# Optimization experiments

Hardware: AMD Instinct MI355X
Metric: run time of the kernel (lower is better)

## Reference

```python
import jax, jax.numpy as jnp
import numpy as np

SAMPLE_RATE = 16000
M = 10          # welch averaging window (frames)
R = 30          # long-term window (frames)
EPS = 1e-5
WIN_LEN = 25    # source bug: ms value used as window length in samples


def _hamming_sq_sum(n):
    # torch.hamming_window(n, periodic=True): 0.54 - 0.46*cos(2*pi*k/n)
    k = np.arange(n)
    w = 0.54 - 0.46 * np.cos(2.0 * np.pi * k / n)
    return np.float32((w ** 2).sum())


def _windowed_mean(x, w):
    """y[:, i, :] = mean(x[:, max(0, i-w):i, :]) for i>=1, y[:,0,:]=0.
    Vectorized via prefix sums: replaces the per-frame Python loop."""
    B, T, F = x.shape
    c = jnp.cumsum(x, axis=1)
    c = jnp.concatenate([jnp.zeros((B, 1, F), x.dtype), c], axis=1)  # c[:, i] = sum of first i frames
    idx = jnp.arange(T)
    lo = jnp.maximum(idx - w, 0)
    cnt = jnp.minimum(idx, w).astype(x.dtype)            # window length per frame (0 at i=0)
    mean = (c[:, idx] - c[:, lo]) / jnp.maximum(cnt, 1)[None, :, None]
    return mean  # mean[:,0,:] == 0 since numerator is 0 there


def setup_inputs() -> dict:
    key = jax.random.key(0)
    x = jax.random.normal(key, (32, 3000, 201, 2), dtype=jnp.float32)
    return {"x": x}


def reference(x) -> jnp.ndarray:
    B, T, F, _ = x.shape
    # speechbrain spectral_magnitude (power=1): power spectrum re^2 + im^2
    spectr = jnp.sum(x * x, axis=-1) / M                         # (B, T, F)
    # welch scaling: /fs * sum(window^2), interior bins doubled
    scale = jnp.ones((F,), x.dtype).at[1:-1].set(2.0)
    s = spectr * (_hamming_sq_sum(WIN_LEN) / SAMPLE_RATE) * scale[None, None, :]
    welch = _windowed_mean(s, M)                                 # (B, T, F)
    # long-term geometric and arithmetic means over R frames of the welch spectrum
    t0 = (jnp.arange(T) == 0)[None, :, None]
    geo = jnp.exp(_windowed_mean(jnp.log(welch + EPS), R)) - EPS
    gm = jnp.where(t0, 0.0, geo) + EPS                           # frame 0 forced to 0 (as in source)
    am = _windowed_mean(welch, R) + EPS
    flatness = -jnp.sum(jnp.log10(gm / am), axis=-1, keepdims=True)  # (B, T, 1)
    return flatness
```

## Files before the change

### kernel.cpp

```cpp
#include <hip/hip_runtime.h>


constexpr int TT = 3000;
constexpr int FF = 201;
constexpr int BB = 32;
constexpr int W1 = 10;
constexpr int W2 = 30;
constexpr int HALO = 40;
constexpr int LTILE = 190;
constexpr int NT = 16;
constexpr int NPROC = 210;
#define EPSV 1e-5f
#define CSCALE (9.935f / 160000.0f)
#define LOG10_2 0.3010299956639812f

#define SUPERGROUP(DYN)                                                        \
  {                                                                            \
            \
    float a0 = 0.f, a1 = 0.f, a2 = 0.f;                                        \
    _Pragma("unroll") for (int j = 0; j < W2; ++j) {                           \
      a0 += w_ring[j]; a1 += l_ring[j];                                        \
    }                                                                          \
    _Pragma("unroll") for (int j = 0; j < W1; ++j) a2 += s_ring[j];            \
    wsum = a0; lsum = a1; ssum = a2;                                           \
    _Pragma("unroll") for (int g = 0; g < 3; ++g) {                            \
                                         \
      _Pragma("unroll") for (int j = 0; j < 10; ++j) {                         \
        int tt = min(tstart + kbase + m0 + (g + 1) * 10 + j, tmax);            \
        nxt[j] = xb[(size_t)tt * FF + f];                                      \
      }                                                                        \
      _Pragma("unroll") for (int j = 0; j < 10; ++j) {                         \
        const int slot30 = g * 10 + j;                                         \
        int m = m0 + g * 10 + j;                                               \
        int t = t0 + m;                                                        \
        float inv10, inv30;                                                    \
        if (DYN) {                                                             \
          inv10 = 1.0f / (float)max(min(t, W1), 1);                            \
          inv30 = 1.0f / (float)max(min(t, W2), 1);                            \
        } else {                                                               \
          inv10 = 0.1f;                                                        \
          inv30 = (1.0f / 30.0f);                                              \
        }                                                                      \
        float welch = ssum * inv10;                                            \
        float lw = __log2f(welch + EPSV);                                      \
        float am = fmaf(wsum, inv30, EPSV);                                    \
        float la = __log2f(am);                                                \
        float contrib = (la - lsum * inv30) * LOG10_2;                         \
        float red = contrib;                                                   \
        _Pragma("unroll") for (int off = 32; off >= 1; off >>= 1)              \
            red += __shfl_xor(red, off, 64);                                   \
        if (lane == 0) part[wv][m] = red;                                      \
                                                            \
        wsum += welch - w_ring[slot30]; w_ring[slot30] = welch;                \
        lsum += lw - l_ring[slot30];    l_ring[slot30] = lw;                   \
                                                                \
        float sv = fmaf(cur[j].x, cur[j].x, cur[j].y * cur[j].y) * cs;         \
        ssum += sv - s_ring[j]; s_ring[j] = sv;                                \
      }                                                                        \
      _Pragma("unroll") for (int j = 0; j < 10; ++j) cur[j] = nxt[j];          \
    }                                                                          \
    m0 += 30;                                                                  \
  }

__global__ __launch_bounds__(256, 2)
void ltsf_kernel(const float2* __restrict__ x, float* __restrict__ out) {
  const int tid = threadIdx.x;
  const int tile = blockIdx.x;
  const int b = blockIdx.y;
  const int t0 = tile * LTILE;
  const bool first = (tile == 0);
  const int tstart = first ? 0 : (t0 - HALO);
  const int lane = tid & 63;
  const int wv = tid >> 6;

  const int f = (tid < FF) ? tid : (FF - 1);
  float cs = (tid < FF) ? ((tid == 0 || tid == FF - 1) ? 1.0f : 2.0f) : 0.0f;
  cs *= CSCALE;

  const float2* xb = x + (size_t)b * TT * FF;
  const int tmax = min(t0 + LTILE, TT) - 1;
  const int validL = min(LTILE, TT - t0);

  __shared__ float part[4][NPROC];

  float s_ring[W1], w_ring[W2], l_ring[W2];
#pragma unroll
  for (int j = 0; j < W1; ++j) s_ring[j] = 0.f;
#pragma unroll
  for (int j = 0; j < W2; ++j) { w_ring[j] = 0.f; l_ring[j] = 0.f; }
  float ssum = 0.f, wsum = 0.f, lsum = 0.f;

  float2 cur[10], nxt[10];

#pragma unroll
  for (int j = 0; j < 10; ++j) {
    int tt = min(tstart + j, tmax);
    cur[j] = xb[(size_t)tt * FF + f];
  }

  const int kbase = first ? 0 : HALO;
  int m0 = 0;

  if (!first) {
    {
#pragma unroll
      for (int j = 0; j < 10; ++j) {
        int tt = min(tstart + 10 + j, tmax);
        nxt[j] = xb[(size_t)tt * FF + f];
      }
#pragma unroll
      for (int j = 0; j < 10; ++j) {
        float sv = fmaf(cur[j].x, cur[j].x, cur[j].y * cur[j].y) * cs;
        ssum += sv;
        s_ring[j] = sv;
      }
#pragma unroll
      for (int j = 0; j < 10; ++j) cur[j] = nxt[j];
    }
#pragma unroll
    for (int g = 0; g < 3; ++g) {
#pragma unroll
      for (int j = 0; j < 10; ++j) {
        int tt = min(tstart + 20 + g * 10 + j, tmax);
        nxt[j] = xb[(size_t)tt * FF + f];
      }
#pragma unroll
      for (int j = 0; j < 10; ++j) {
        const int slot30 = g * 10 + j;
        float welch = ssum * 0.1f;
        float lw = __log2f(welch + EPSV);
        wsum += welch; w_ring[slot30] = welch;
        lsum += lw;    l_ring[slot30] = lw;
        float sv = fmaf(cur[j].x, cur[j].x, cur[j].y * cur[j].y) * cs;
        ssum += sv - s_ring[j];
        s_ring[j] = sv;
      }
#pragma unroll
      for (int j = 0; j < 10; ++j) cur[j] = nxt[j];
    }
  }

  if (first) {
    SUPERGROUP(true);
    for (int sg = 1; sg < 7; ++sg) {
      if (m0 >= validL) break;
      SUPERGROUP(false);
    }
  } else {
    for (int sg = 0; sg < 7; ++sg) {
      if (m0 >= validL) break;
      SUPERGROUP(false);
    }
  }

  __syncthreads();
  if (tid < validL) {
    float v = part[0][tid] + part[1][tid] + part[2][tid] + part[3][tid];
    if (first && tid == 0) v = 0.f;
    out[(size_t)b * TT + t0 + tid] = v;
  }
}

extern "C" void kernel_launch(void* const* d_in, const int* in_sizes, int n_in,
                              void* d_out, int out_size, void* d_ws, size_t ws_size,
                              hipStream_t stream) {
  const float2* x = (const float2*)d_in[0];
  float* out = (float*)d_out;
  dim3 grid(NT, BB);
  ltsf_kernel<<<grid, 256, 0, stream>>>(x, out);
}
```

Measured before the change: 242.8 us.

## Shrink time tiles to 60 frames, batch wave reductions, raise occupancy

Splits the time axis into 50 tiles of 60 frames instead of 16 tiles of 190, which gives 1600 blocks instead of 512 and fully unrolls the fixed two supergroups per tile. The per-frame wave shuffle reductions are batched ten at a time so the shuffles can be interleaved, and the launch bound asks for 4 blocks per CU. The cost is a 40-frame halo on each much shorter tile, so redundant loads and recompute rise to about two thirds of the useful work, and register pressure may constrain the higher occupancy target.

```diff
diff --git a/kernel.cpp b/kernel.cpp
--- a/kernel.cpp
+++ b/kernel.cpp
@@ -7,9 +7,8 @@
 constexpr int W1 = 10;
 constexpr int W2 = 30;
 constexpr int HALO = 40;
-constexpr int LTILE = 190;
-constexpr int NT = 16;
-constexpr int NPROC = 210;
+constexpr int LTILE = 60;
+constexpr int NT = 50;
 #define EPSV 1e-5f
 #define CSCALE (9.935f / 160000.0f)
 #define LOG10_2 0.3010299956639812f
@@ -29,10 +28,11 @@
         int tt = min(tstart + kbase + m0 + (g + 1) * 10 + j, tmax);            \
         nxt[j] = xb[(size_t)tt * FF + f];                                      \
       }                                                                        \
+      float rr[10];                                                            \
+                   \
       _Pragma("unroll") for (int j = 0; j < 10; ++j) {                         \
         const int slot30 = g * 10 + j;                                         \
-        int m = m0 + g * 10 + j;                                               \
-        int t = t0 + m;                                                        \
+        int t = t0 + m0 + g * 10 + j;                                          \
         float inv10, inv30;                                                    \
         if (DYN) {                                                             \
           inv10 = 1.0f / (float)max(min(t, W1), 1);                            \
@@ -45,24 +45,27 @@
         float lw = __log2f(welch + EPSV);                                      \
         float am = fmaf(wsum, inv30, EPSV);                                    \
         float la = __log2f(am);                                                \
-        float contrib = (la - lsum * inv30) * LOG10_2;                         \
-        float red = contrib;                                                   \
-        _Pragma("unroll") for (int off = 32; off >= 1; off >>= 1)              \
-            red += __shfl_xor(red, off, 64);                                   \
-        if (lane == 0) part[wv][m] = red;                                      \
-                                                            \
+        rr[j] = (la - lsum * inv30) * LOG10_2;                                 \
         wsum += welch - w_ring[slot30]; w_ring[slot30] = welch;                \
         lsum += lw - l_ring[slot30];    l_ring[slot30] = lw;                   \
-                                                                \
         float sv = fmaf(cur[j].x, cur[j].x, cur[j].y * cur[j].y) * cs;         \
         ssum += sv - s_ring[j]; s_ring[j] = sv;                                \
+      }                                                                        \
+                 \
+      _Pragma("unroll") for (int off = 32; off >= 1; off >>= 1) {              \
+        _Pragma("unroll") for (int j = 0; j < 10; ++j)                         \
+            rr[j] += __shfl_xor(rr[j], off, 64);                               \
+      }                                                                        \
+      if (lane == 0) {                                                         \
+        _Pragma("unroll") for (int j = 0; j < 10; ++j)                         \
+            part[wv][m0 + g * 10 + j] = rr[j];                                 \
       }                                                                        \
       _Pragma("unroll") for (int j = 0; j < 10; ++j) cur[j] = nxt[j];          \
     }                                                                          \
     m0 += 30;                                                                  \
   }
 
-__global__ __launch_bounds__(256, 2)
+__global__ __launch_bounds__(256, 4)
 void ltsf_kernel(const float2* __restrict__ x, float* __restrict__ out) {
   const int tid = threadIdx.x;
   const int tile = blockIdx.x;
@@ -78,10 +81,9 @@
   cs *= CSCALE;
 
   const float2* xb = x + (size_t)b * TT * FF;
-  const int tmax = min(t0 + LTILE, TT) - 1;
-  const int validL = min(LTILE, TT - t0);
+  const int tmax = t0 + LTILE - 1;
 
-  __shared__ float part[4][NPROC];
+  __shared__ float part[4][LTILE];
 
   float s_ring[W1], w_ring[W2], l_ring[W2];
 #pragma unroll
@@ -142,19 +144,14 @@
 
   if (first) {
     SUPERGROUP(true);
-    for (int sg = 1; sg < 7; ++sg) {
-      if (m0 >= validL) break;
-      SUPERGROUP(false);
-    }
+    SUPERGROUP(false);
   } else {
-    for (int sg = 0; sg < 7; ++sg) {
-      if (m0 >= validL) break;
-      SUPERGROUP(false);
-    }
+    SUPERGROUP(false);
+    SUPERGROUP(false);
   }
 
   __syncthreads();
-  if (tid < validL) {
+  if (tid < LTILE) {
     float v = part[0][tid] + part[1][tid] + part[2][tid] + part[3][tid];
     if (first && tid == 0) v = 0.f;
     out[(size_t)b * TT + t0 + tid] = v;
```

Result: no change. 244.7 us (+0.8%).
